# Kernel optimization log

Hardware: AMD Instinct MI355X
Metric: run time of the kernel (lower is better)

## Reference

```python
import jax, jax.numpy as jnp
import numpy as np

TEMPERATURE = 1.0  # module default current_temperature
TOP_K = 2
NUM_EXPERTS = 64
EPS = 1e-10


def setup_inputs() -> dict:
    key = jax.random.key(0)
    k1, k2 = jax.random.split(key)
    x = jax.random.normal(k1, (4, 4096, 2048), dtype=jnp.float32)
    # nn.Linear(d_model, num_experts) weight has shape [num_experts, d_model]
    W_gate = jax.random.normal(k2, (NUM_EXPERTS, 2048), dtype=jnp.float32) * (1.0 / np.sqrt(2048))
    return {"x": x, "W_gate": W_gate}


def reference(x, W_gate):
    # Gate GEMM: [B,S,D] x [E,D] -> [B,S,E]
    logits = jnp.einsum("bsd,ed->bse", x, W_gate)
    scaled = logits / TEMPERATURE
    # Full distribution over experts (for load-balancing loss)
    router_probs = jax.nn.softmax(scaled, axis=-1)
    # Top-k selection over the expert dim, then renormalize via softmax
    top_k_logits, top_k_indices = jax.lax.top_k(scaled, TOP_K)  # [B,S,K]
    top_k_weights = jax.nn.softmax(top_k_logits, axis=-1)
    # Routing stats (no-grad in torch; plain values here)
    entropy = -jnp.sum(router_probs * jnp.log(router_probs + EPS), axis=-1)
    routing_entropy = entropy.mean()
    selection_confidence = top_k_weights[:, :, 0].mean()
    counts = jnp.zeros((NUM_EXPERTS,), dtype=x.dtype).at[top_k_indices.reshape(-1)].add(1.0)
    expert_utilization = counts / (counts.sum() + EPS)
    return (top_k_weights, top_k_indices, router_probs,
            routing_entropy, selection_confidence, expert_utilization)
```

## Files before the change

kernel.cpp:

```cpp
#include <hip/hip_runtime.h>
#include <math.h>

#define NTOK 16384
#define DIM 2048
#define NEXP 64
#define BT 64
#define KC 32
#define NSTAGE (DIM / KC)

#define OFF_W    0
#define OFF_I    32768
#define OFF_P    65536
#define OFF_ENT  1114112
#define OFF_CONF 1114113
#define OFF_UTIL 1114114

typedef short s16x8 __attribute__((ext_vector_type(8)));
typedef float f32x4 __attribute__((ext_vector_type(4)));

__device__ __forceinline__ unsigned short f2bf(float v) {
    unsigned u = __builtin_bit_cast(unsigned, v);
    u = u + 0x7FFFu + ((u >> 16) & 1u);
    return (unsigned short)(u >> 16);
}
__device__ __forceinline__ float bf2f(unsigned short b) {
    return __builtin_bit_cast(float, (unsigned)b << 16);
}

__global__ void router_init(float* __restrict__ out) {
    int tid = threadIdx.x;
    if (tid < 66) out[OFF_ENT + tid] = 0.0f;
}

__global__ void router_wsplit(const float* __restrict__ Wg, uint4* __restrict__ wsp) {
    const int c = blockIdx.x;
    const int t = threadIdx.x;
    const int nt = t >> 6, l = t & 63;
    const int e  = 16 * nt + (l & 15);
    const int k0 = 32 * c + 8 * (l >> 4);
    const float* src = Wg + (size_t)e * DIM + k0;
    float4 a = *(const float4*)src;
    float4 b = *(const float4*)(src + 4);
    float v[8] = {a.x, a.y, a.z, a.w, b.x, b.y, b.z, b.w};
    unsigned short H[8], M[8], L[8];
    #pragma unroll
    for (int j = 0; j < 8; ++j) {
        H[j] = f2bf(v[j]);  float r = v[j] - bf2f(H[j]);
        M[j] = f2bf(r);     r = r - bf2f(M[j]);
        L[j] = f2bf(r);
    }
    uint4 ph, pm, pl;
    ph.x = H[0] | ((unsigned)H[1] << 16); ph.y = H[2] | ((unsigned)H[3] << 16);
    ph.z = H[4] | ((unsigned)H[5] << 16); ph.w = H[6] | ((unsigned)H[7] << 16);
    pm.x = M[0] | ((unsigned)M[1] << 16); pm.y = M[2] | ((unsigned)M[3] << 16);
    pm.z = M[4] | ((unsigned)M[5] << 16); pm.w = M[6] | ((unsigned)M[7] << 16);
    pl.x = L[0] | ((unsigned)L[1] << 16); pl.y = L[2] | ((unsigned)L[3] << 16);
    pl.z = L[4] | ((unsigned)L[5] << 16); pl.w = L[6] | ((unsigned)L[7] << 16);
    const int idx = c * 256 + t;
    wsp[idx]             = ph;
    wsp[16384 + idx]     = pm;
    wsp[32768 + idx]     = pl;
}

#define LOADX(p_, c_) { xset##p_[0] = xq[8*(c_) + 2*qd]; xset##p_[1] = xq[8*(c_) + 2*qd + 1]; }
#define LOADW(p_, c_) { wset##p_[0] = wq[(c_)*256 + tid];          \
                        wset##p_[1] = wq[16384 + (c_)*256 + tid];  \
                        wset##p_[2] = wq[32768 + (c_)*256 + tid]; }
#define STOREW(p_, bf_) { *(uint4*)&Bs[0][bf_][wv][l8] = wset##p_[0];  \
                          *(uint4*)&Bs[1][bf_][wv][l8] = wset##p_[1];  \
                          *(uint4*)&Bs[2][bf_][wv][l8] = wset##p_[2]; }
#define CONVX(p_) {                                                     \
    float xv[8];                                                        \
    xv[0]=xset##p_[0].x; xv[1]=xset##p_[0].y; xv[2]=xset##p_[0].z; xv[3]=xset##p_[0].w; \
    xv[4]=xset##p_[1].x; xv[5]=xset##p_[1].y; xv[6]=xset##p_[1].z; xv[7]=xset##p_[1].w; \
    _Pragma("unroll")                                                   \
    for (int j = 0; j < 8; ++j) {                                       \
        unsigned short h_ = f2bf(xv[j]); float r_ = xv[j] - bf2f(h_);   \
        unsigned short m_ = f2bf(r_);    r_ = r_ - bf2f(m_);            \
        unsigned short s_ = f2bf(r_);                                   \
        ah[j] = (short)h_; am[j] = (short)m_; al[j] = (short)s_;        \
    } }
#define COMPUTE(bf_) {                                                  \
    _Pragma("unroll")                                                   \
    for (int nt = 0; nt < 4; ++nt) {                                    \
        s16x8 bh_ = *(const s16x8*)&Bs[0][bf_][nt][l8];                 \
        s16x8 bm_ = *(const s16x8*)&Bs[1][bf_][nt][l8];                 \
        s16x8 bl_ = *(const s16x8*)&Bs[2][bf_][nt][l8];                 \
        acc[nt] = __builtin_amdgcn_mfma_f32_16x16x32_bf16(ah, bh_, acc[nt], 0, 0, 0); \
        acc[nt] = __builtin_amdgcn_mfma_f32_16x16x32_bf16(am, bh_, acc[nt], 0, 0, 0); \
        acc[nt] = __builtin_amdgcn_mfma_f32_16x16x32_bf16(ah, bm_, acc[nt], 0, 0, 0); \
        acc[nt] = __builtin_amdgcn_mfma_f32_16x16x32_bf16(am, bm_, acc[nt], 0, 0, 0); \
        acc[nt] = __builtin_amdgcn_mfma_f32_16x16x32_bf16(ah, bl_, acc[nt], 0, 0, 0); \
        acc[nt] = __builtin_amdgcn_mfma_f32_16x16x32_bf16(al, bh_, acc[nt], 0, 0, 0); \
    } }

__global__ __launch_bounds__(256, 1) void router_main(
    const float* __restrict__ x, const uint4* __restrict__ wq,
    float* __restrict__ out)
{
    __shared__ __align__(16) unsigned short Bs[3][2][4][512];
    __shared__ float lg[BT][NEXP + 1];
    __shared__ float m1s[BT], rss[BT];
    __shared__ float s_ent, s_conf, s_cnt[NEXP];

    const int tid = threadIdx.x;
    const int l   = tid & 63;
    const int wv  = tid >> 6;
    const int qd  = l >> 4;
    const int l8  = l * 8;
    const int t0  = blockIdx.x * BT;

    if (tid == 0) { s_ent = 0.0f; s_conf = 0.0f; }
    if (tid < NEXP) s_cnt[tid] = 0.0f;

    const float4* xq = (const float4*)(x + (size_t)(t0 + 16 * wv + (l & 15)) * DIM);

    f32x4 acc[4];
    #pragma unroll
    for (int nt = 0; nt < 4; ++nt) acc[nt] = (f32x4)(0.0f);

    s16x8 ah, am, al;
    float4 xset0[2], xset1[2];
    uint4  wset0[3], wset1[3];

    LOADX(0, 0); LOADX(1, 1);
    LOADW(0, 0); LOADW(1, 1);
    STOREW(0, 0);
    __syncthreads();

    for (int c = 0; c < NSTAGE; c += 2) {
        CONVX(0);
        if (c + 2 < NSTAGE) { LOADX(0, c + 2); LOADW(0, c + 2); }
        COMPUTE(0);
        STOREW(1, 1);
        __syncthreads();
        CONVX(1);
        if (c + 3 < NSTAGE) { LOADX(1, c + 3); LOADW(1, c + 3); }
        COMPUTE(1);
        if (c + 2 < NSTAGE) STOREW(0, 0);
        __syncthreads();
    }

    #pragma unroll
    for (int nt = 0; nt < 4; ++nt)
        #pragma unroll
        for (int r = 0; r < 4; ++r)
            lg[16 * wv + 4 * qd + r][16 * nt + (l & 15)] = acc[nt][r];
    __syncthreads();

    if (tid < BT) {
        const int t = tid;
        float m1 = -INFINITY, m2 = -INFINITY;
        int i1 = 0, i2 = 0;
        for (int e = 0; e < NEXP; ++e) {
            float lv = lg[t][e];
            if (lv > m1)      { m2 = m1; i2 = i1; m1 = lv; i1 = e; }
            else if (lv > m2) { m2 = lv; i2 = e; }
        }
        float ssum = 0.0f, tsum = 0.0f;
        for (int e = 0; e < NEXP; ++e) {
            float d = lg[t][e] - m1;
            float ex = __expf(d);
            ssum += ex;
            tsum += d * ex;
        }
        float rs = 1.0f / ssum;
        float H  = logf(ssum) - tsum * rs;
        float e2 = __expf(m2 - m1);
        float rn = 1.0f / (1.0f + e2);
        float w0 = rn, w1v = e2 * rn;
        m1s[t] = m1; rss[t] = rs;

        *(float2*)&out[OFF_W + 2 * (t0 + t)] = make_float2(w0, w1v);
        *(float2*)&out[OFF_I + 2 * (t0 + t)] = make_float2((float)i1, (float)i2);

        atomicAdd(&s_ent,  H);
        atomicAdd(&s_conf, w0);
        atomicAdd(&s_cnt[i1], 1.0f);
        atomicAdd(&s_cnt[i2], 1.0f);
    }
    __syncthreads();

    #pragma unroll
    for (int p = 0; p < 4; ++p) {
        int Q  = tid + 256 * p;
        int t  = Q >> 4;
        int qq = Q & 15;
        float m  = m1s[t];
        float rs = rss[t];
        float4 pr;
        pr.x = __expf(lg[t][4 * qq + 0] - m) * rs;
        pr.y = __expf(lg[t][4 * qq + 1] - m) * rs;
        pr.z = __expf(lg[t][4 * qq + 2] - m) * rs;
        pr.w = __expf(lg[t][4 * qq + 3] - m) * rs;
        *(float4*)&out[OFF_P + (size_t)(t0 + t) * NEXP + 4 * qq] = pr;
    }

    if (tid == 0) {
        atomicAdd(&out[OFF_ENT],  s_ent  * (1.0f / 16384.0f));
        atomicAdd(&out[OFF_CONF], s_conf * (1.0f / 16384.0f));
    }
    if (tid < NEXP)
        atomicAdd(&out[OFF_UTIL + tid], s_cnt[tid] * (1.0f / 32768.0f));
}

extern "C" void kernel_launch(void* const* d_in, const int* in_sizes, int n_in,
                              void* d_out, int out_size, void* d_ws, size_t ws_size,
                              hipStream_t stream) {
    const float* x  = (const float*)d_in[0];
    const float* Wg = (const float*)d_in[1];
    float* out = (float*)d_out;
    (void)in_sizes; (void)n_in; (void)out_size; (void)ws_size;

    router_init<<<dim3(1), dim3(128), 0, stream>>>(out);
    router_wsplit<<<dim3(NSTAGE), dim3(256), 0, stream>>>(Wg, (uint4*)d_ws);
    router_main<<<dim3(NTOK / BT), dim3(256), 0, stream>>>(x, (const uint4*)d_ws, out);
}
```

Baseline: 273.9 us.

## Use 16-token blocks with per-wave expert tiles and direct-register weight loads

The token block shrinks from 64 to 16 and each wave now owns one 16-expert tile, loading its bf16-split weights straight from global memory into registers. This removes the LDS staging of the weights and the two barriers per stage, and launches four times as many blocks with a higher occupancy hint. The x split now uses truncation masks instead of round-to-nearest, and the six MFMAs alternate between two accumulators to shorten the dependency chain. In exchange, all four waves in a block read the same 16 x rows, so each x row is loaded four times instead of once, which raises traffic on the memory-bound input.

```diff
diff --git a/kernel.cpp b/kernel.cpp
--- a/kernel.cpp
+++ b/kernel.cpp
@@ -4,7 +4,7 @@
 #define NTOK 16384
 #define DIM 2048
 #define NEXP 64
-#define BT 64
+#define TB 16
 #define KC 32
 #define NSTAGE (DIM / KC)
 
@@ -57,98 +57,90 @@
     pl.x = L[0] | ((unsigned)L[1] << 16); pl.y = L[2] | ((unsigned)L[3] << 16);
     pl.z = L[4] | ((unsigned)L[5] << 16); pl.w = L[6] | ((unsigned)L[7] << 16);
     const int idx = c * 256 + t;
-    wsp[idx]             = ph;
-    wsp[16384 + idx]     = pm;
-    wsp[32768 + idx]     = pl;
+    wsp[idx]         = ph;
+    wsp[16384 + idx] = pm;
+    wsp[32768 + idx] = pl;
 }
 
 #define LOADX(p_, c_) { xset##p_[0] = xq[8*(c_) + 2*qd]; xset##p_[1] = xq[8*(c_) + 2*qd + 1]; }
-#define LOADW(p_, c_) { wset##p_[0] = wq[(c_)*256 + tid];          \
-                        wset##p_[1] = wq[16384 + (c_)*256 + tid];  \
-                        wset##p_[2] = wq[32768 + (c_)*256 + tid]; }
-#define STOREW(p_, bf_) { *(uint4*)&Bs[0][bf_][wv][l8] = wset##p_[0];  \
-                          *(uint4*)&Bs[1][bf_][wv][l8] = wset##p_[1];  \
-                          *(uint4*)&Bs[2][bf_][wv][l8] = wset##p_[2]; }
-#define CONVX(p_) {                                                     \
-    float xv[8];                                                        \
+#define LOADW(p_, c_) { const int idx_ = (c_)*256 + wv*64 + l;  \
+                        wset##p_[0] = wq[idx_];                 \
+                        wset##p_[1] = wq[16384 + idx_];         \
+                        wset##p_[2] = wq[32768 + idx_]; }
+
+#define CONVX(p_) {                                                      \
+    float xv[8];                                                         \
     xv[0]=xset##p_[0].x; xv[1]=xset##p_[0].y; xv[2]=xset##p_[0].z; xv[3]=xset##p_[0].w; \
     xv[4]=xset##p_[1].x; xv[5]=xset##p_[1].y; xv[6]=xset##p_[1].z; xv[7]=xset##p_[1].w; \
-    _Pragma("unroll")                                                   \
-    for (int j = 0; j < 8; ++j) {                                       \
-        unsigned short h_ = f2bf(xv[j]); float r_ = xv[j] - bf2f(h_);   \
-        unsigned short m_ = f2bf(r_);    r_ = r_ - bf2f(m_);            \
-        unsigned short s_ = f2bf(r_);                                   \
-        ah[j] = (short)h_; am[j] = (short)m_; al[j] = (short)s_;        \
+    _Pragma("unroll")                                                    \
+    for (int j = 0; j < 8; ++j) {                                        \
+        unsigned u_  = __builtin_bit_cast(unsigned, xv[j]);              \
+        unsigned hb_ = u_ & 0xFFFF0000u;                                 \
+        float    r_  = xv[j] - __builtin_bit_cast(float, hb_);           \
+        unsigned mb_ = __builtin_bit_cast(unsigned, r_) & 0xFFFF0000u;   \
+        float    r2_ = r_ - __builtin_bit_cast(float, mb_);              \
+        unsigned lb_ = __builtin_bit_cast(unsigned, r2_);                \
+        ah[j] = (short)(hb_ >> 16);                                      \
+        am[j] = (short)(mb_ >> 16);                                      \
+        al[j] = (short)(lb_ >> 16);                                      \
     } }
-#define COMPUTE(bf_) {                                                  \
-    _Pragma("unroll")                                                   \
-    for (int nt = 0; nt < 4; ++nt) {                                    \
-        s16x8 bh_ = *(const s16x8*)&Bs[0][bf_][nt][l8];                 \
-        s16x8 bm_ = *(const s16x8*)&Bs[1][bf_][nt][l8];                 \
-        s16x8 bl_ = *(const s16x8*)&Bs[2][bf_][nt][l8];                 \
-        acc[nt] = __builtin_amdgcn_mfma_f32_16x16x32_bf16(ah, bh_, acc[nt], 0, 0, 0); \
-        acc[nt] = __builtin_amdgcn_mfma_f32_16x16x32_bf16(am, bh_, acc[nt], 0, 0, 0); \
-        acc[nt] = __builtin_amdgcn_mfma_f32_16x16x32_bf16(ah, bm_, acc[nt], 0, 0, 0); \
-        acc[nt] = __builtin_amdgcn_mfma_f32_16x16x32_bf16(am, bm_, acc[nt], 0, 0, 0); \
-        acc[nt] = __builtin_amdgcn_mfma_f32_16x16x32_bf16(ah, bl_, acc[nt], 0, 0, 0); \
-        acc[nt] = __builtin_amdgcn_mfma_f32_16x16x32_bf16(al, bh_, acc[nt], 0, 0, 0); \
-    } }
-
-__global__ __launch_bounds__(256, 1) void router_main(
+
+#define COMPUTE(p_) {                                                    \
+    s16x8 bh_ = __builtin_bit_cast(s16x8, wset##p_[0]);                  \
+    s16x8 bm_ = __builtin_bit_cast(s16x8, wset##p_[1]);                  \
+    s16x8 bl_ = __builtin_bit_cast(s16x8, wset##p_[2]);                  \
+    acc0 = __builtin_amdgcn_mfma_f32_16x16x32_bf16(ah, bh_, acc0, 0, 0, 0); \
+    acc1 = __builtin_amdgcn_mfma_f32_16x16x32_bf16(am, bh_, acc1, 0, 0, 0); \
+    acc0 = __builtin_amdgcn_mfma_f32_16x16x32_bf16(ah, bm_, acc0, 0, 0, 0); \
+    acc1 = __builtin_amdgcn_mfma_f32_16x16x32_bf16(am, bm_, acc1, 0, 0, 0); \
+    acc0 = __builtin_amdgcn_mfma_f32_16x16x32_bf16(ah, bl_, acc0, 0, 0, 0); \
+    acc1 = __builtin_amdgcn_mfma_f32_16x16x32_bf16(al, bh_, acc1, 0, 0, 0); \
+    }
+
+__global__ __launch_bounds__(256, 4) void router_main(
     const float* __restrict__ x, const uint4* __restrict__ wq,
     float* __restrict__ out)
 {
-    __shared__ __align__(16) unsigned short Bs[3][2][4][512];
-    __shared__ float lg[BT][NEXP + 1];
-    __shared__ float m1s[BT], rss[BT];
+    __shared__ float lg[TB][NEXP + 1];
+    __shared__ float m1s[TB], rss[TB];
     __shared__ float s_ent, s_conf, s_cnt[NEXP];
 
     const int tid = threadIdx.x;
     const int l   = tid & 63;
-    const int wv  = tid >> 6;
+    const int wv  = __builtin_amdgcn_readfirstlane(tid >> 6);
     const int qd  = l >> 4;
-    const int l8  = l * 8;
-    const int t0  = blockIdx.x * BT;
+    const int t0  = blockIdx.x * TB;
 
     if (tid == 0) { s_ent = 0.0f; s_conf = 0.0f; }
     if (tid < NEXP) s_cnt[tid] = 0.0f;
 
-    const float4* xq = (const float4*)(x + (size_t)(t0 + 16 * wv + (l & 15)) * DIM);
-
-    f32x4 acc[4];
-    #pragma unroll
-    for (int nt = 0; nt < 4; ++nt) acc[nt] = (f32x4)(0.0f);
-
+    const float4* xq = (const float4*)(x + (size_t)(t0 + (l & 15)) * DIM);
+
+    f32x4 acc0 = (f32x4)(0.0f), acc1 = (f32x4)(0.0f);
     s16x8 ah, am, al;
     float4 xset0[2], xset1[2];
     uint4  wset0[3], wset1[3];
 
     LOADX(0, 0); LOADX(1, 1);
     LOADW(0, 0); LOADW(1, 1);
-    STOREW(0, 0);
-    __syncthreads();
 
     for (int c = 0; c < NSTAGE; c += 2) {
         CONVX(0);
-        if (c + 2 < NSTAGE) { LOADX(0, c + 2); LOADW(0, c + 2); }
+        if (c + 2 < NSTAGE) LOADX(0, c + 2);
         COMPUTE(0);
-        STOREW(1, 1);
-        __syncthreads();
+        if (c + 2 < NSTAGE) LOADW(0, c + 2);
         CONVX(1);
-        if (c + 3 < NSTAGE) { LOADX(1, c + 3); LOADW(1, c + 3); }
+        if (c + 3 < NSTAGE) LOADX(1, c + 3);
         COMPUTE(1);
-        if (c + 2 < NSTAGE) STOREW(0, 0);
-        __syncthreads();
+        if (c + 3 < NSTAGE) LOADW(1, c + 3);
     }
 
     #pragma unroll
-    for (int nt = 0; nt < 4; ++nt)
-        #pragma unroll
-        for (int r = 0; r < 4; ++r)
-            lg[16 * wv + 4 * qd + r][16 * nt + (l & 15)] = acc[nt][r];
+    for (int r = 0; r < 4; ++r)
+        lg[4 * qd + r][16 * wv + (l & 15)] = acc0[r] + acc1[r];
     __syncthreads();
 
-    if (tid < BT) {
+    if (tid < TB) {
         const int t = tid;
         float m1 = -INFINITY, m2 = -INFINITY;
         int i1 = 0, i2 = 0;
@@ -181,11 +173,9 @@
     }
     __syncthreads();
 
-    #pragma unroll
-    for (int p = 0; p < 4; ++p) {
-        int Q  = tid + 256 * p;
-        int t  = Q >> 4;
-        int qq = Q & 15;
+    {
+        int t  = tid >> 4;
+        int qq = tid & 15;
         float m  = m1s[t];
         float rs = rss[t];
         float4 pr;
@@ -214,5 +204,5 @@
 
     router_init<<<dim3(1), dim3(128), 0, stream>>>(out);
     router_wsplit<<<dim3(NSTAGE), dim3(256), 0, stream>>>(Wg, (uint4*)d_ws);
-    router_main<<<dim3(NTOK / BT), dim3(256), 0, stream>>>(x, (const uint4*)d_ws, out);
-}
+    router_main<<<dim3(NTOK / TB), dim3(256), 0, stream>>>(x, (const uint4*)d_ws, out);
+}
```

New measurement: 281.3 us. 1.03x slower.
